# Optimization experiments

Measured on AMD Instinct MI355X. Metric: run time of the kernel, lower is better.

## Reference

```python
import jax, jax.numpy as jnp
import numpy as np

B, G, S, C = 64, 2048, 64, 3


def setup_inputs() -> dict:
    key = jax.random.key(0)
    k1, k2 = jax.random.split(key)
    neighbor = jax.random.normal(k1, (B, G, S, C), dtype=jnp.float32)
    center = jax.random.normal(k2, (B, G, C), dtype=jnp.float32)
    return {"neighbor": neighbor, "center": center}


def _disambiguate_vector_directions(lps, vecs):
    # lps: [B,G,S,3] local points; vecs: [B,G,3] candidate axes.
    knn = lps.shape[2]
    proj = jnp.sum(vecs[:, :, None, :] * lps, axis=3)                 # [B,G,S]
    n_pos = jnp.sum((proj > 0).astype(jnp.float32), axis=2, keepdims=True)  # [B,G,1]
    flip = (n_pos < 0.5 * knn).astype(jnp.float32)
    return (1.0 - 2.0 * flip) * vecs


def reference(neighbor, center):
    # neighbor: [B,G,S,3] (C==3 path -> axis1/axis2 both PCA)
    pos = neighbor[..., 0:3]
    # Distance-based weights for weighted PCA covariance.
    norms = jnp.linalg.norm(pos, axis=3, keepdims=True)               # [B,G,S,1]
    max_norms = jnp.max(norms, axis=2, keepdims=True)                 # [B,G,1,1]
    w = max_norms - norms
    w = w / (jnp.sum(w, axis=2, keepdims=True) + 1e-6)
    scaled_pos = 100.0 * pos
    # Weighted covariance: [B,G,3,3]
    covs = jnp.einsum('bgsk,bgsl->bgkl', w * scaled_pos, scaled_pos)
    # Symmetric 3x3 eigendecomposition, eigenvalues ascending, eigenvectors as columns
    # (same convention as pytorch3d symeig3x3; signs fixed by disambiguation below).
    _, eigvec = jnp.linalg.eigh(covs)                                 # [B,G,3,3]
    z_axis = _disambiguate_vector_directions(pos, eigvec[:, :, :, 0])  # smallest-eig
    x_axis = _disambiguate_vector_directions(pos, eigvec[:, :, :, 2])  # largest-eig
    y_axis = jnp.cross(z_axis, x_axis)                                # [B,G,3]
    lrfs = jnp.stack((z_axis, y_axis, x_axis), axis=3)                # [B,G,3,3] (columns)
    # Rotate local points into the LRF: batched [S,3] x [3,3]
    rot_neighbor = jnp.einsum('bgsc,bgcd->bgsd', pos, lrfs)           # [B,G,S,3]
    return (rot_neighbor, lrfs)
```

## Files before the change

### kernel.cpp

```cpp
#include <hip/hip_runtime.h>
#include <math.h>


__device__ __forceinline__ float slapy2_(float x, float y) {
    _Pragma("clang fp contract(off)")
    float xa = fabsf(x), ya = fabsf(y);
    float w = fmaxf(xa, ya), z = fminf(xa, ya);
    if (z == 0.0f) return w;
    float t = z / w;
    return w * sqrtf(1.0f + t * t);
}

__device__ __forceinline__ void slartg_(float f, float g,
                                        float &c, float &s, float &r) {
    _Pragma("clang fp contract(off)")
    if (g == 0.0f) { c = 1.0f; s = 0.0f; r = f; return; }
    if (f == 0.0f) { c = 0.0f; s = (g >= 0.0f) ? 1.0f : -1.0f; r = fabsf(g); return; }
    float d = sqrtf(f * f + g * g);
    float p = 1.0f / d;
    c = fabsf(f) * p;
    s = g * ((f >= 0.0f) ? p : -p);
    r = (f >= 0.0f) ? d : -d;
}

__device__ __forceinline__ void slaev2_(float a, float b, float cc,
                                        float &rt1, float &rt2,
                                        float &cs1, float &sn1) {
    _Pragma("clang fp contract(off)")
    float sm = a + cc, df = a - cc;
    float adf = fabsf(df);
    float tb = b + b;
    float ab = fabsf(tb);
    float acmx, acmn;
    if (fabsf(a) > fabsf(cc)) { acmx = a; acmn = cc; } else { acmx = cc; acmn = a; }
    float rt;
    if (adf > ab)      { float t = ab / adf; rt = adf * sqrtf(1.0f + t * t); }
    else if (adf < ab) { float t = adf / ab; rt = ab * sqrtf(1.0f + t * t); }
    else                rt = ab * sqrtf(2.0f);
    int sgn1;
    if (sm < 0.0f)      { rt1 = 0.5f * (sm - rt); sgn1 = -1; rt2 = (acmx / rt1) * acmn - (b / rt1) * b; }
    else if (sm > 0.0f) { rt1 = 0.5f * (sm + rt); sgn1 =  1; rt2 = (acmx / rt1) * acmn - (b / rt1) * b; }
    else                { rt1 = 0.5f * rt; rt2 = -0.5f * rt; sgn1 = 1; }
    int sgn2;
    float cs;
    if (df >= 0.0f) { cs = df + rt; sgn2 = 1; } else { cs = df - rt; sgn2 = -1; }
    float acs = fabsf(cs);
    if (acs > ab) {
        float ct = -tb / cs;
        sn1 = 1.0f / sqrtf(1.0f + ct * ct);
        cs1 = ct * sn1;
    } else {
        if (ab == 0.0f) { cs1 = 1.0f; sn1 = 0.0f; }
        else {
            float tn = -cs / tb;
            cs1 = 1.0f / sqrtf(1.0f + tn * tn);
            sn1 = tn * cs1;
        }
    }
    if (sgn1 == sgn2) { float tn = cs1; cs1 = -sn1; sn1 = tn; }
}

__device__ __forceinline__ float getd3(int i, float d1, float d2, float d3) {
    return (i == 1) ? d1 : ((i == 2) ? d2 : d3);
}
__device__ __forceinline__ void setd3(int i, float v, float &d1, float &d2, float &d3) {
    d1 = (i == 1) ? v : d1;
    d2 = (i == 2) ? v : d2;
    d3 = (i == 3) ? v : d3;
}
__device__ __forceinline__ float gete2(int i, float e1, float e2) {
    return (i == 1) ? e1 : e2;
}
__device__ __forceinline__ void sete2(int i, float v, float &e1, float &e2) {
    e1 = (i == 1) ? v : e1;
    e2 = (i == 2) ? v : e2;
}

__device__ __forceinline__ void zrot3r(int j, float ctemp, float stemp,
                                       float &z11, float &z12, float &z13,
                                       float &z21, float &z22, float &z23,
                                       float &z31, float &z32, float &z33) {
    _Pragma("clang fp contract(off)")
    if (j == 1) {
        { float t = z12; z12 = (ctemp * t) - (stemp * z11); z11 = (stemp * t) + (ctemp * z11); }
        { float t = z22; z22 = (ctemp * t) - (stemp * z21); z21 = (stemp * t) + (ctemp * z21); }
        { float t = z32; z32 = (ctemp * t) - (stemp * z31); z31 = (stemp * t) + (ctemp * z31); }
    } else {
        { float t = z13; z13 = (ctemp * t) - (stemp * z12); z12 = (stemp * t) + (ctemp * z12); }
        { float t = z23; z23 = (ctemp * t) - (stemp * z22); z22 = (stemp * t) + (ctemp * z22); }
        { float t = z33; z33 = (ctemp * t) - (stemp * z32); z32 = (stemp * t) + (ctemp * z32); }
    }
}

__device__ __forceinline__ void ssteqr3_reg(
        float &d1_, float &d2_, float &d3_, float &e1_, float &e2_,
        float &z11, float &z12, float &z13,
        float &z21, float &z22, float &z23,
        float &z31, float &z32, float &z33) {
    _Pragma("clang fp contract(off)")
    const float EPS    = 5.9604644775390625e-8f;
    const float EPS2   = EPS * EPS;
    const float SAFMIN = 1.17549435e-38f;
    const int n = 3, nmaxit = 3 * 30;
    int jtot = 0, l1 = 1;

#define GD(i)      getd3((i), d1_, d2_, d3_)
#define SD(i, v)   setd3((i), (v), d1_, d2_, d3_)
#define GE(i)      gete2((i), e1_, e2_)
#define SE(i, v)   sete2((i), (v), e1_, e2_)
#define ZR(j, c, s) zrot3r((j), (c), (s), z11, z12, z13, z21, z22, z23, z31, z32, z33)

    while (true) {
        if (l1 > n) break;
        if (l1 > 1) SE(l1 - 1, 0.0f);
        int m = n;
        for (int mm = l1; mm <= n - 1; ++mm) {
            float tst = fabsf(GE(mm));
            if (tst == 0.0f) { m = mm; break; }
            if (tst <= (sqrtf(fabsf(GD(mm))) * sqrtf(fabsf(GD(mm + 1)))) * EPS) {
                SE(mm, 0.0f); m = mm; break;
            }
        }
        int l = l1, lsv = l, lend = m, lendsv = lend;
        l1 = m + 1;
        if (lend == l) continue;
        if (fabsf(GD(lend)) < fabsf(GD(l))) { lend = lsv; l = lendsv; }

        if (lend > l) {
            while (true) {
                m = lend;
                if (l != lend) {
                    for (int mm = l; mm <= lend - 1; ++mm) {
                        float em = GE(mm);
                        float tst = em * em;
                        if (tst <= (EPS2 * fabsf(GD(mm))) * fabsf(GD(mm + 1)) + SAFMIN) { m = mm; break; }
                    }
                }
                if (m < lend) SE(m, 0.0f);
                float p = GD(l);
                if (m == l) {
                    SD(l, p); ++l;
                    if (l <= lend) continue;
                    break;
                }
                if (m == l + 1) {
                    float rt1, rt2, c, s;
                    slaev2_(GD(l), GE(l), GD(l + 1), rt1, rt2, c, s);
                    ZR(l, c, s);
                    SD(l, rt1); SD(l + 1, rt2); SE(l, 0.0f);
                    l += 2;
                    if (l <= lend) continue;
                    break;
                }
                if (jtot == nmaxit) break;
                ++jtot;
                {
                    float el = GE(l);
                    float g = (GD(l + 1) - p) / (2.0f * el);
                    float r = slapy2_(g, 1.0f);
                    g = GD(m) - p + el / (g + ((g >= 0.0f) ? r : -r));
                    float s = 1.0f, c = 1.0f;
                    p = 0.0f;
                    for (int i = m - 1; i >= l; --i) {
                        float ei = GE(i);
                        float f = s * ei;
                        float b = c * ei;
                        slartg_(g, f, c, s, r);
                        if (i != m - 1) SE(i + 1, r);
                        g = GD(i + 1) - p;
                        float r2 = ((GD(i) - g) * s) + ((2.0f * c) * b);
                        p = s * r2;
                        SD(i + 1, g + p);
                        g = (c * r2) - b;
                        ZR(i, c, -s);
                    }
                    SD(l, GD(l) - p);
                    SE(l, g);
                }
            }
        } else if (lend < l) {
            while (true) {
                m = lend;
                if (l != lend) {
                    for (int mm = l; mm >= lend + 1; --mm) {
                        float em = GE(mm - 1);
                        float tst = em * em;
                        if (tst <= (EPS2 * fabsf(GD(mm))) * fabsf(GD(mm - 1)) + SAFMIN) { m = mm; break; }
                    }
                }
                if (m > lend) SE(m - 1, 0.0f);
                float p = GD(l);
                if (m == l) {
                    SD(l, p); --l;
                    if (l >= lend) continue;
                    break;
                }
                if (m == l - 1) {
                    float rt1, rt2, c, s;
                    slaev2_(GD(l - 1), GE(l - 1), GD(l), rt1, rt2, c, s);
                    ZR(l - 1, c, s);
                    SD(l - 1, rt1); SD(l, rt2); SE(l - 1, 0.0f);
                    l -= 2;
                    if (l >= lend) continue;
                    break;
                }
                if (jtot == nmaxit) break;
                ++jtot;
                {
                    float el = GE(l - 1);
                    float g = (GD(l - 1) - p) / (2.0f * el);
                    float r = slapy2_(g, 1.0f);
                    g = GD(m) - p + el / (g + ((g >= 0.0f) ? r : -r));
                    float s = 1.0f, c = 1.0f;
                    p = 0.0f;
                    for (int i = m; i <= l - 1; ++i) {
                        float ei = GE(i);
                        float f = s * ei;
                        float b = c * ei;
                        slartg_(g, f, c, s, r);
                        if (i != m) SE(i - 1, r);
                        g = GD(i) - p;
                        float r2 = ((GD(i + 1) - g) * s) + ((2.0f * c) * b);
                        p = s * r2;
                        SD(i, g + p);
                        g = (c * r2) - b;
                        ZR(i, c, s);
                    }
                    SD(l, GD(l) - p);
                    SE(l - 1, g);
                }
            }
        }
    }
    {
        int k = 1; float p = d1_;
        if (d2_ < p) { k = 2; p = d2_; }
        if (d3_ < p) { k = 3; p = d3_; }
        if (k == 2) {
            d2_ = d1_; d1_ = p;
            float t;
            t = z11; z11 = z12; z12 = t;
            t = z21; z21 = z22; z22 = t;
            t = z31; z31 = z32; z32 = t;
        } else if (k == 3) {
            d3_ = d1_; d1_ = p;
            float t;
            t = z11; z11 = z13; z13 = t;
            t = z21; z21 = z23; z23 = t;
            t = z31; z31 = z33; z33 = t;
        }
        if (d3_ < d2_) {
            float t = d2_; d2_ = d3_; d3_ = t;
            t = z12; z12 = z13; z13 = t;
            t = z22; z22 = z23; z23 = t;
            t = z32; z32 = z33; z33 = t;
        }
    }
#undef GD
#undef SD
#undef GE
#undef SE
#undef ZR
}

__device__ __forceinline__ float nrm3_(float x, float y, float z) {
    _Pragma("clang fp contract(off)")
    float t = (x * x) + (y * y);
    t = t + (z * z);
    return sqrtf(t);
}

__device__ __forceinline__ void covstep(float px, float py, float pz, float wq,
                                        float &c00, float &c10, float &c20,
                                        float &c11, float &c21, float &c22) {
    _Pragma("clang fp contract(off)")
    const float spx = 100.0f * px, spy = 100.0f * py, spz = 100.0f * pz;
    const float ax = wq * spx, ay = wq * spy, az = wq * spz;
    c00 = c00 + (ax * spx);
    c10 = c10 + (ay * spx);
    c20 = c20 + (az * spx);
    c11 = c11 + (ay * spy);
    c21 = c21 + (az * spy);
    c22 = c22 + (az * spz);
}

__device__ __forceinline__ void projstep(float px, float py, float pz,
                                         float zv0, float zv1, float zv2,
                                         float xv0, float xv1, float xv2,
                                         int &cz, int &cx) {
    _Pragma("clang fp contract(off)")
    const float pjz = ((zv0 * px) + (zv1 * py)) + (zv2 * pz);
    const float pjx = ((xv0 * px) + (xv1 * py)) + (xv2 * pz);
    cz += (pjz > 0.0f) ? 1 : 0;
    cx += (pjx > 0.0f) ? 1 : 0;
}

__device__ __forceinline__ void rotstep(float px, float py, float pz,
                                        float zv0, float zv1, float zv2,
                                        float yv0, float yv1, float yv2,
                                        float xv0, float xv1, float xv2,
                                        float sz, float sy, float sx,
                                        float &ra, float &rb, float &rc) {
    _Pragma("clang fp contract(off)")
    ra = (((px * zv0) + (py * zv1)) + (pz * zv2)) * sz;
    rb = (((px * yv0) + (py * yv1)) + (pz * yv2)) * sy;
    rc = (((px * xv0) + (py * xv1)) + (pz * xv2)) * sx;
}

__global__ __launch_bounds__(256, 8) void lrf_kernel(const float* __restrict__ nbr,
                                                     float* __restrict__ rot,
                                                     float* __restrict__ lrf) {
    _Pragma("clang fp contract(off)")
    __shared__ float wql[64 * 65];
    __shared__ float cov6[64 * 7];
    const int tid = threadIdx.x;
    const int gl  = tid >> 2;
    const int k   = tid & 3;
    const int g   = (blockIdx.x << 6) + gl;
    const int lbase = gl * 65;

    const float4* __restrict__ p4 = reinterpret_cast<const float4*>(nbr)
                                    + (long long)g * 48 + k * 12;
    const float4* __restrict__ q4 = reinterpret_cast<const float4*>(nbr)
                                    + (long long)g * 48;

    float mx = -3.402823466e+38f;
#pragma unroll
    for (int q = 0; q < 4; ++q) {
        const float4 v0 = p4[q * 3 + 0];
        const float4 v1 = p4[q * 3 + 1];
        const float4 v2 = p4[q * 3 + 2];
        const float n0 = nrm3_(v0.x, v0.y, v0.z);
        const float n1 = nrm3_(v0.w, v1.x, v1.y);
        const float n2 = nrm3_(v1.z, v1.w, v2.x);
        const float n3 = nrm3_(v2.y, v2.z, v2.w);
        const int b = lbase + 16 * k + 4 * q;
        wql[b + 0] = n0;
        wql[b + 1] = n1;
        wql[b + 2] = n2;
        wql[b + 3] = n3;
        mx = fmaxf(mx, fmaxf(fmaxf(n0, n1), fmaxf(n2, n3)));
    }
    mx = fmaxf(mx, __shfl_xor(mx, 1, 64));
    mx = fmaxf(mx, __shfl_xor(mx, 2, 64));
    __builtin_amdgcn_wave_barrier();
    asm volatile("" ::: "memory");

    float r0_ = 0.0f, r1_ = 0.0f;
    {
        const int j0 = lbase + 2 * k;
#pragma unroll
        for (int t = 0; t < 8; ++t) {
            r0_ = r0_ + (mx - wql[j0 + 8 * t + 0]);
            r1_ = r1_ + (mx - wql[j0 + 8 * t + 1]);
        }
    }
    const float A_ = r0_ + r1_;
    const float B_ = A_ + __shfl_xor(A_, 1, 64);
    const float ws = B_ + __shfl_xor(B_, 2, 64);
    const float denom = ws + 1e-6f;
    asm volatile("" ::: "memory");

#pragma unroll
    for (int i = 0; i < 16; ++i) {
        const int idx = lbase + 16 * k + i;
        const float nv = wql[idx];
        wql[idx] = (mx - nv) / denom;
    }
    __builtin_amdgcn_wave_barrier();
    asm volatile("" ::: "memory");

    float c00 = 0.0f, c10 = 0.0f, c20 = 0.0f, c11 = 0.0f, c21 = 0.0f, c22 = 0.0f;
#pragma unroll 4
    for (int q = 0; q < 16; ++q) {
        const float4 v0 = q4[q * 3 + 0];
        const float4 v1 = q4[q * 3 + 1];
        const float4 v2 = q4[q * 3 + 2];
        const float w0 = wql[lbase + 4 * q + 0];
        const float w1 = wql[lbase + 4 * q + 1];
        const float w2 = wql[lbase + 4 * q + 2];
        const float w3 = wql[lbase + 4 * q + 3];
        covstep(v0.x, v0.y, v0.z, w0, c00, c10, c20, c11, c21, c22);
        covstep(v0.w, v1.x, v1.y, w1, c00, c10, c20, c11, c21, c22);
        covstep(v1.z, v1.w, v2.x, w2, c00, c10, c20, c11, c21, c22);
        covstep(v2.y, v2.z, v2.w, w3, c00, c10, c20, c11, c21, c22);
    }

    {
        const float vA = (k == 0) ? c00 : ((k == 1) ? c10 : ((k == 2) ? c20 : c11));
        cov6[gl * 7 + k] = vA;
        if (k < 2) {
            const float vB = (k == 0) ? c21 : c22;
            cov6[gl * 7 + 4 + k] = vB;
        }
    }
    __syncthreads();

    if (tid < 64) {
        const int tb = tid * 7;
        const float a11 = cov6[tb + 0];
        const float a21 = cov6[tb + 1];
        const float a31 = cov6[tb + 2];
        const float a22 = cov6[tb + 3];
        const float a32 = cov6[tb + 4];
        const float a33 = cov6[tb + 5];

        float taui, v2h, e1q, d2q, d3q, e2q;
        const float xnorm = fabsf(a31);
        if (xnorm == 0.0f) {
            taui = 0.0f; v2h = a31; e1q = a21; d2q = a22; e2q = a32; d3q = a33;
        } else {
            const float beta = -copysignf(slapy2_(a21, xnorm), a21);
            taui = (beta - a21) / beta;
            const float rcp = 1.0f / (a21 - beta);
            v2h = a31 * rcp;
            e1q = beta;
            float x1 = taui * a22;
            float x2 = taui * a32;
            const float temp2 = a32 * v2h;
            x1 = x1 + (taui * temp2);
            const float t1v = taui * v2h;
            x2 = x2 + (t1v * a33);
            const float dt = x1 + (x2 * v2h);
            const float alpha_c = (-0.5f * taui) * dt;
            const float w1 = x1 + alpha_c;
            const float w2 = x2 + (alpha_c * v2h);
            d2q = (a22 - w1) - w1;
            e2q = (a32 - (v2h * w1)) - w2;
            d3q = (a33 - (v2h * w2)) - (w2 * v2h);
        }

        float d1_ = a11, d2_ = d2q, d3_ = d3q, e1_ = e1q, e2_ = e2q;
        float z11 = 1.0f, z12 = 0.0f, z13 = 0.0f;
        float z21 = 0.0f, z22 = 1.0f, z23 = 0.0f;
        float z31 = 0.0f, z32 = 0.0f, z33 = 1.0f;
        ssteqr3_reg(d1_, d2_, d3_, e1_, e2_,
                    z11, z12, z13, z21, z22, z23, z31, z32, z33);

        float zv0, zv1, zv2, xv0, xv1, xv2;
        {
            const float u2 = z21, u3 = z31;
            zv0 = z11;
            if (taui != 0.0f) {
                const float wj = u2 + (u3 * v2h);
                const float pj = taui * wj;
                zv1 = u2 - pj;
                zv2 = u3 - (v2h * pj);
            } else { zv1 = u2; zv2 = u3; }
        }
        {
            const float u2 = z23, u3 = z33;
            xv0 = z13;
            if (taui != 0.0f) {
                const float wj = u2 + (u3 * v2h);
                const float pj = taui * wj;
                xv1 = u2 - pj;
                xv2 = u3 - (v2h * pj);
            } else { xv1 = u2; xv2 = u3; }
        }

        wql[tb + 0] = zv0;
        wql[tb + 1] = zv1;
        wql[tb + 2] = zv2;
        wql[tb + 3] = xv0;
        wql[tb + 4] = xv1;
        wql[tb + 5] = xv2;
    }
    __syncthreads();

    const int ab = gl * 7;
    const float zv0 = wql[ab + 0], zv1 = wql[ab + 1], zv2 = wql[ab + 2];
    const float xv0 = wql[ab + 3], xv1 = wql[ab + 4], xv2 = wql[ab + 5];

    const float yv0 = (zv1 * xv2) - (zv2 * xv1);
    const float yv1 = (zv2 * xv0) - (zv0 * xv2);
    const float yv2 = (zv0 * xv1) - (zv1 * xv0);

    int cz = 0, cx = 0;
#pragma unroll
    for (int q = 0; q < 4; ++q) {
        const float4 v0 = p4[q * 3 + 0];
        const float4 v1 = p4[q * 3 + 1];
        const float4 v2 = p4[q * 3 + 2];
        projstep(v0.x, v0.y, v0.z, zv0, zv1, zv2, xv0, xv1, xv2, cz, cx);
        projstep(v0.w, v1.x, v1.y, zv0, zv1, zv2, xv0, xv1, xv2, cz, cx);
        projstep(v1.z, v1.w, v2.x, zv0, zv1, zv2, xv0, xv1, xv2, cz, cx);
        projstep(v2.y, v2.z, v2.w, zv0, zv1, zv2, xv0, xv1, xv2, cz, cx);
    }
    cz += __shfl_xor(cz, 1, 64);
    cz += __shfl_xor(cz, 2, 64);
    cx += __shfl_xor(cx, 1, 64);
    cx += __shfl_xor(cx, 2, 64);
    const float sz = (cz < 32) ? -1.0f : 1.0f;
    const float sx = (cx < 32) ? -1.0f : 1.0f;
    const float sy = sz * sx;

    float4* __restrict__ o4 = reinterpret_cast<float4*>(rot)
                              + (long long)g * 48 + k * 12;
#pragma unroll
    for (int q = 0; q < 4; ++q) {
        const float4 v0 = p4[q * 3 + 0];
        const float4 v1 = p4[q * 3 + 1];
        const float4 v2 = p4[q * 3 + 2];
        float r0a, r0b, r0c, r1a, r1b, r1c, r2a, r2b, r2c, r3a, r3b, r3c;
        rotstep(v0.x, v0.y, v0.z, zv0, zv1, zv2, yv0, yv1, yv2, xv0, xv1, xv2,
                sz, sy, sx, r0a, r0b, r0c);
        rotstep(v0.w, v1.x, v1.y, zv0, zv1, zv2, yv0, yv1, yv2, xv0, xv1, xv2,
                sz, sy, sx, r1a, r1b, r1c);
        rotstep(v1.z, v1.w, v2.x, zv0, zv1, zv2, yv0, yv1, yv2, xv0, xv1, xv2,
                sz, sy, sx, r2a, r2b, r2c);
        rotstep(v2.y, v2.z, v2.w, zv0, zv1, zv2, yv0, yv1, yv2, xv0, xv1, xv2,
                sz, sy, sx, r3a, r3b, r3c);
        float4 o0, o1, o2;
        o0.x = r0a; o0.y = r0b; o0.z = r0c; o0.w = r1a;
        o1.x = r1b; o1.y = r1c; o1.z = r2a; o1.w = r2b;
        o2.x = r2c; o2.y = r3a; o2.z = r3b; o2.w = r3c;
        o4[q * 3 + 0] = o0;
        o4[q * 3 + 1] = o1;
        o4[q * 3 + 2] = o2;
    }

    if (k < 3) {
        const float zc = ((k == 0) ? zv0 : ((k == 1) ? zv1 : zv2)) * sz;
        const float yc = ((k == 0) ? yv0 : ((k == 1) ? yv1 : yv2)) * sy;
        const float xc = ((k == 0) ? xv0 : ((k == 1) ? xv1 : xv2)) * sx;
        float* __restrict__ lp = lrf + (long long)g * 9 + 3 * k;
        lp[0] = zc;
        lp[1] = yc;
        lp[2] = xc;
    }
}

extern "C" void kernel_launch(void* const* d_in, const int* in_sizes, int n_in,
                              void* d_out, int out_size, void* d_ws, size_t ws_size,
                              hipStream_t stream) {
    const float* neighbor = (const float*)d_in[0];
    float* rot = (float*)d_out;
    float* lrf = (float*)d_out + (long long)64 * 2048 * 64 * 3;

    lrf_kernel<<<dim3(2048), dim3(256), 0, stream>>>(neighbor, rot, lrf);
}
```

Baseline: 334.6 us.

## Keep neighbor points in registers and exchange via wave shuffles instead of LDS

Restructures the kernel to one wave per block handling 16 groups, caching each thread's 16 points in registers so the input is read from global memory once instead of being re-read for the covariance, projection and rotation passes. Shared memory and __syncthreads are replaced by cross-lane shuffles for the weight sum, the covariance accumulation and the broadcast of the eigenvectors. The cost is many more shuffle instructions (four per point per source lane in the covariance loop), higher register pressure, and an eigen solve that occupies only 16 of 64 lanes.

Result: faster. 312.1 us (-6.7%).

```diff
diff --git a/kernel.cpp b/kernel.cpp
--- a/kernel.cpp
+++ b/kernel.cpp
@@ -307,104 +307,95 @@
     rc = (((px * xv0) + (py * xv1)) + (pz * xv2)) * sx;
 }
 
-__global__ __launch_bounds__(256, 8) void lrf_kernel(const float* __restrict__ nbr,
-                                                     float* __restrict__ rot,
-                                                     float* __restrict__ lrf) {
-    _Pragma("clang fp contract(off)")
-    __shared__ float wql[64 * 65];
-    __shared__ float cov6[64 * 7];
-    const int tid = threadIdx.x;
-    const int gl  = tid >> 2;
-    const int k   = tid & 3;
-    const int g   = (blockIdx.x << 6) + gl;
-    const int lbase = gl * 65;
+__global__ __launch_bounds__(64, 4) void lrf_kernel(const float* __restrict__ nbr,
+                                                    float* __restrict__ rot,
+                                                    float* __restrict__ lrf) {
+    _Pragma("clang fp contract(off)")
+    const int lane = threadIdx.x;
+    const int gl   = lane >> 2;
+    const int k    = lane & 3;
+    const int g    = (blockIdx.x << 4) + gl;
+    const int cb   = lane & 60;
 
     const float4* __restrict__ p4 = reinterpret_cast<const float4*>(nbr)
                                     + (long long)g * 48 + k * 12;
-    const float4* __restrict__ q4 = reinterpret_cast<const float4*>(nbr)
-                                    + (long long)g * 48;
-
+
+    float px[16], py[16], pz[16], wv[16];
     float mx = -3.402823466e+38f;
 #pragma unroll
     for (int q = 0; q < 4; ++q) {
         const float4 v0 = p4[q * 3 + 0];
         const float4 v1 = p4[q * 3 + 1];
         const float4 v2 = p4[q * 3 + 2];
-        const float n0 = nrm3_(v0.x, v0.y, v0.z);
-        const float n1 = nrm3_(v0.w, v1.x, v1.y);
-        const float n2 = nrm3_(v1.z, v1.w, v2.x);
-        const float n3 = nrm3_(v2.y, v2.z, v2.w);
-        const int b = lbase + 16 * k + 4 * q;
-        wql[b + 0] = n0;
-        wql[b + 1] = n1;
-        wql[b + 2] = n2;
-        wql[b + 3] = n3;
+        px[4 * q + 0] = v0.x; py[4 * q + 0] = v0.y; pz[4 * q + 0] = v0.z;
+        px[4 * q + 1] = v0.w; py[4 * q + 1] = v1.x; pz[4 * q + 1] = v1.y;
+        px[4 * q + 2] = v1.z; py[4 * q + 2] = v1.w; pz[4 * q + 2] = v2.x;
+        px[4 * q + 3] = v2.y; py[4 * q + 3] = v2.z; pz[4 * q + 3] = v2.w;
+        const float n0 = nrm3_(px[4 * q + 0], py[4 * q + 0], pz[4 * q + 0]);
+        const float n1 = nrm3_(px[4 * q + 1], py[4 * q + 1], pz[4 * q + 1]);
+        const float n2 = nrm3_(px[4 * q + 2], py[4 * q + 2], pz[4 * q + 2]);
+        const float n3 = nrm3_(px[4 * q + 3], py[4 * q + 3], pz[4 * q + 3]);
+        wv[4 * q + 0] = n0; wv[4 * q + 1] = n1;
+        wv[4 * q + 2] = n2; wv[4 * q + 3] = n3;
         mx = fmaxf(mx, fmaxf(fmaxf(n0, n1), fmaxf(n2, n3)));
     }
     mx = fmaxf(mx, __shfl_xor(mx, 1, 64));
     mx = fmaxf(mx, __shfl_xor(mx, 2, 64));
-    __builtin_amdgcn_wave_barrier();
-    asm volatile("" ::: "memory");
-
-    float r0_ = 0.0f, r1_ = 0.0f;
+
+    float R[8];
+#pragma unroll
+    for (int j = 0; j < 8; ++j) {
+        const float wj  = mx - wv[j];
+        const float wj8 = mx - wv[j + 8];
+        R[j] = wj + wj8;
+    }
+#pragma unroll
+    for (int step = 1; step <= 3; ++step) {
+#pragma unroll
+        for (int j = 0; j < 8; ++j) {
+            const float T  = __shfl(R[j], cb + (step - 1), 64);
+            const float wj  = mx - wv[j];
+            const float wj8 = mx - wv[j + 8];
+            const float R2 = (T + wj) + wj8;
+            R[j] = (k == step) ? R2 : R[j];
+        }
+    }
+    float denom;
     {
-        const int j0 = lbase + 2 * k;
-#pragma unroll
-        for (int t = 0; t < 8; ++t) {
-            r0_ = r0_ + (mx - wql[j0 + 8 * t + 0]);
-            r1_ = r1_ + (mx - wql[j0 + 8 * t + 1]);
-        }
-    }
-    const float A_ = r0_ + r1_;
-    const float B_ = A_ + __shfl_xor(A_, 1, 64);
-    const float ws = B_ + __shfl_xor(B_, 2, 64);
-    const float denom = ws + 1e-6f;
-    asm volatile("" ::: "memory");
+        const float ws = ((R[0] + R[1]) + (R[2] + R[3]))
+                       + ((R[4] + R[5]) + (R[6] + R[7]));
+        denom = __shfl(ws + 1e-6f, cb + 3, 64);
+    }
 
 #pragma unroll
     for (int i = 0; i < 16; ++i) {
-        const int idx = lbase + 16 * k + i;
-        const float nv = wql[idx];
-        wql[idx] = (mx - nv) / denom;
-    }
-    __builtin_amdgcn_wave_barrier();
-    asm volatile("" ::: "memory");
+        wv[i] = (mx - wv[i]) / denom;
+    }
 
     float c00 = 0.0f, c10 = 0.0f, c20 = 0.0f, c11 = 0.0f, c21 = 0.0f, c22 = 0.0f;
-#pragma unroll 4
-    for (int q = 0; q < 16; ++q) {
-        const float4 v0 = q4[q * 3 + 0];
-        const float4 v1 = q4[q * 3 + 1];
-        const float4 v2 = q4[q * 3 + 2];
-        const float w0 = wql[lbase + 4 * q + 0];
-        const float w1 = wql[lbase + 4 * q + 1];
-        const float w2 = wql[lbase + 4 * q + 2];
-        const float w3 = wql[lbase + 4 * q + 3];
-        covstep(v0.x, v0.y, v0.z, w0, c00, c10, c20, c11, c21, c22);
-        covstep(v0.w, v1.x, v1.y, w1, c00, c10, c20, c11, c21, c22);
-        covstep(v1.z, v1.w, v2.x, w2, c00, c10, c20, c11, c21, c22);
-        covstep(v2.y, v2.z, v2.w, w3, c00, c10, c20, c11, c21, c22);
-    }
-
-    {
-        const float vA = (k == 0) ? c00 : ((k == 1) ? c10 : ((k == 2) ? c20 : c11));
-        cov6[gl * 7 + k] = vA;
-        if (k < 2) {
-            const float vB = (k == 0) ? c21 : c22;
-            cov6[gl * 7 + 4 + k] = vB;
-        }
-    }
-    __syncthreads();
-
-    if (tid < 64) {
-        const int tb = tid * 7;
-        const float a11 = cov6[tb + 0];
-        const float a21 = cov6[tb + 1];
-        const float a31 = cov6[tb + 2];
-        const float a22 = cov6[tb + 3];
-        const float a32 = cov6[tb + 4];
-        const float a33 = cov6[tb + 5];
-
+    for (int o = 0; o < 4; ++o) {
+        const int src = cb + o;
+#pragma unroll
+        for (int i = 0; i < 16; ++i) {
+            const float bx  = __shfl(px[i], src, 64);
+            const float by  = __shfl(py[i], src, 64);
+            const float bz  = __shfl(pz[i], src, 64);
+            const float wqs = __shfl(wv[i], src, 64);
+            covstep(bx, by, bz, wqs, c00, c10, c20, c11, c21, c22);
+        }
+    }
+
+    const int covSrc = (lane & 15) << 2;
+    const float a11 = __shfl(c00, covSrc, 64);
+    const float a21 = __shfl(c10, covSrc, 64);
+    const float a31 = __shfl(c20, covSrc, 64);
+    const float a22 = __shfl(c11, covSrc, 64);
+    const float a32 = __shfl(c21, covSrc, 64);
+    const float a33 = __shfl(c22, covSrc, 64);
+
+    float zv0e = 0.0f, zv1e = 0.0f, zv2e = 0.0f;
+    float xv0e = 0.0f, xv1e = 0.0f, xv2e = 0.0f;
+    if (lane < 16) {
         float taui, v2h, e1q, d2q, d3q, e2q;
         const float xnorm = fabsf(a31);
         if (xnorm == 0.0f) {
@@ -437,40 +428,34 @@
         ssteqr3_reg(d1_, d2_, d3_, e1_, e2_,
                     z11, z12, z13, z21, z22, z23, z31, z32, z33);
 
-        float zv0, zv1, zv2, xv0, xv1, xv2;
         {
             const float u2 = z21, u3 = z31;
-            zv0 = z11;
+            zv0e = z11;
             if (taui != 0.0f) {
                 const float wj = u2 + (u3 * v2h);
                 const float pj = taui * wj;
-                zv1 = u2 - pj;
-                zv2 = u3 - (v2h * pj);
-            } else { zv1 = u2; zv2 = u3; }
+                zv1e = u2 - pj;
+                zv2e = u3 - (v2h * pj);
+            } else { zv1e = u2; zv2e = u3; }
         }
         {
             const float u2 = z23, u3 = z33;
-            xv0 = z13;
+            xv0e = z13;
             if (taui != 0.0f) {
                 const float wj = u2 + (u3 * v2h);
                 const float pj = taui * wj;
-                xv1 = u2 - pj;
-                xv2 = u3 - (v2h * pj);
-            } else { xv1 = u2; xv2 = u3; }
-        }
-
-        wql[tb + 0] = zv0;
-        wql[tb + 1] = zv1;
-        wql[tb + 2] = zv2;
-        wql[tb + 3] = xv0;
-        wql[tb + 4] = xv1;
-        wql[tb + 5] = xv2;
-    }
-    __syncthreads();
-
-    const int ab = gl * 7;
-    const float zv0 = wql[ab + 0], zv1 = wql[ab + 1], zv2 = wql[ab + 2];
-    const float xv0 = wql[ab + 3], xv1 = wql[ab + 4], xv2 = wql[ab + 5];
+                xv1e = u2 - pj;
+                xv2e = u3 - (v2h * pj);
+            } else { xv1e = u2; xv2e = u3; }
+        }
+    }
+
+    const float zv0 = __shfl(zv0e, gl, 64);
+    const float zv1 = __shfl(zv1e, gl, 64);
+    const float zv2 = __shfl(zv2e, gl, 64);
+    const float xv0 = __shfl(xv0e, gl, 64);
+    const float xv1 = __shfl(xv1e, gl, 64);
+    const float xv2 = __shfl(xv2e, gl, 64);
 
     const float yv0 = (zv1 * xv2) - (zv2 * xv1);
     const float yv1 = (zv2 * xv0) - (zv0 * xv2);
@@ -478,14 +463,8 @@
 
     int cz = 0, cx = 0;
 #pragma unroll
-    for (int q = 0; q < 4; ++q) {
-        const float4 v0 = p4[q * 3 + 0];
-        const float4 v1 = p4[q * 3 + 1];
-        const float4 v2 = p4[q * 3 + 2];
-        projstep(v0.x, v0.y, v0.z, zv0, zv1, zv2, xv0, xv1, xv2, cz, cx);
-        projstep(v0.w, v1.x, v1.y, zv0, zv1, zv2, xv0, xv1, xv2, cz, cx);
-        projstep(v1.z, v1.w, v2.x, zv0, zv1, zv2, xv0, xv1, xv2, cz, cx);
-        projstep(v2.y, v2.z, v2.w, zv0, zv1, zv2, xv0, xv1, xv2, cz, cx);
+    for (int i = 0; i < 16; ++i) {
+        projstep(px[i], py[i], pz[i], zv0, zv1, zv2, xv0, xv1, xv2, cz, cx);
     }
     cz += __shfl_xor(cz, 1, 64);
     cz += __shfl_xor(cz, 2, 64);
@@ -499,17 +478,18 @@
                               + (long long)g * 48 + k * 12;
 #pragma unroll
     for (int q = 0; q < 4; ++q) {
-        const float4 v0 = p4[q * 3 + 0];
-        const float4 v1 = p4[q * 3 + 1];
-        const float4 v2 = p4[q * 3 + 2];
         float r0a, r0b, r0c, r1a, r1b, r1c, r2a, r2b, r2c, r3a, r3b, r3c;
-        rotstep(v0.x, v0.y, v0.z, zv0, zv1, zv2, yv0, yv1, yv2, xv0, xv1, xv2,
+        rotstep(px[4 * q + 0], py[4 * q + 0], pz[4 * q + 0],
+                zv0, zv1, zv2, yv0, yv1, yv2, xv0, xv1, xv2,
                 sz, sy, sx, r0a, r0b, r0c);
-        rotstep(v0.w, v1.x, v1.y, zv0, zv1, zv2, yv0, yv1, yv2, xv0, xv1, xv2,
+        rotstep(px[4 * q + 1], py[4 * q + 1], pz[4 * q + 1],
+                zv0, zv1, zv2, yv0, yv1, yv2, xv0, xv1, xv2,
                 sz, sy, sx, r1a, r1b, r1c);
-        rotstep(v1.z, v1.w, v2.x, zv0, zv1, zv2, yv0, yv1, yv2, xv0, xv1, xv2,
+        rotstep(px[4 * q + 2], py[4 * q + 2], pz[4 * q + 2],
+                zv0, zv1, zv2, yv0, yv1, yv2, xv0, xv1, xv2,
                 sz, sy, sx, r2a, r2b, r2c);
-        rotstep(v2.y, v2.z, v2.w, zv0, zv1, zv2, yv0, yv1, yv2, xv0, xv1, xv2,
+        rotstep(px[4 * q + 3], py[4 * q + 3], pz[4 * q + 3],
+                zv0, zv1, zv2, yv0, yv1, yv2, xv0, xv1, xv2,
                 sz, sy, sx, r3a, r3b, r3c);
         float4 o0, o1, o2;
         o0.x = r0a; o0.y = r0b; o0.z = r0c; o0.w = r1a;
@@ -538,5 +518,5 @@
     float* rot = (float*)d_out;
     float* lrf = (float*)d_out + (long long)64 * 2048 * 64 * 3;
 
-    lrf_kernel<<<dim3(2048), dim3(256), 0, stream>>>(neighbor, rot, lrf);
-}
+    lrf_kernel<<<dim3(8192), dim3(64), 0, stream>>>(neighbor, rot, lrf);
+}
```
